# Optimization experiments

Measured on AMD Instinct MI355X. Metric: run time of the kernel, lower is better.

## Reference

```python
import jax, jax.numpy as jnp
import numpy as np

B, S, D, K = 64, 2048, 192, 128  # batch, seq, projection_dim, memoryBankSize


def setup_inputs() -> dict:
    key = jax.random.key(0)
    k1, k2, k3 = jax.random.split(key, 3)
    return {
        "projections": jax.random.normal(k1, (B, S, D), jnp.float32),
        "mem_bank": jax.random.normal(k2, (K, D), jnp.float32),
        "glu_w": jax.random.normal(k3, (D, 2 * D), jnp.float32) * 0.05,
        "glu_b": jnp.zeros((2 * D,), jnp.float32),
    }


def _l2_normalize(x, axis):
    # matches tf.math.l2_normalize (eps inside the max under the sqrt)
    sq = jnp.sum(x * x, axis=axis, keepdims=True)
    return x / jnp.sqrt(jnp.maximum(sq, 1e-12))


def _sinkhorn(out):
    # out: [K, N] cosine similarities
    Q = jnp.exp(out / 0.05)
    Kf = jnp.asarray(Q.shape[0], Q.dtype)
    Bf = jnp.asarray(Q.shape[1], Q.dtype)
    Q = Q / jnp.sum(Q)
    for _ in range(3):  # fixed 3 iterations, as in source
        Q = Q / (jnp.sum(Q, axis=1, keepdims=True) * Kf)  # row normalize
        Q = Q / (jnp.sum(Q, axis=0, keepdims=True) * Bf)  # col normalize
    return Q * Bf


def reference(projections, mem_bank, glu_w, glu_b):
    Bsz, Ssz, Dd = projections.shape
    x = projections.reshape(-1, Dd)                      # [N, D]
    proj_n = _l2_normalize(x, axis=1)                    # [N, D]
    mem_n = _l2_normalize(mem_bank, axis=1)              # [K, D]
    sim = jnp.einsum('kd,nd->kn', mem_n, proj_n)         # [K, N]
    Q = _sinkhorn(sim)                                   # [K, N]
    # top_k(Q^T, 1) per token == argmax over codebook axis
    idx = jnp.argmax(Q, axis=0)                          # [N] int
    assign = mem_bank[idx]                               # gather, [N, D]
    # GLU: Dense(2D) then value * sigmoid(gate)
    lin = assign @ glu_w + glu_b                         # [N, 2D]
    gated = lin[:, :Dd] * jax.nn.sigmoid(lin[:, Dd:])    # [N, D]
    # reduce_mean over the stacked pair == average
    return (projections + gated.reshape(Bsz, Ssz, Dd)) * 0.5
```

## Files before the change

### kernel.cpp

```cpp
#include <hip/hip_runtime.h>

#define NTOK  131072
#define DDIM  192
#define KMEM  128
#define TWOD  384
#define GBLK  2048

typedef _Float16 half8 __attribute__((ext_vector_type(8)));
typedef float   floatx4 __attribute__((ext_vector_type(4)));

__device__ __forceinline__ int swz(int row, int h) {
  return row * DDIM + ((((h >> 3) ^ (row & 7)) << 3));
}

__global__ __launch_bounds__(192) void prep_kernel(
    const float* __restrict__ mb, const float* __restrict__ W,
    const float* __restrict__ bias, _Float16* __restrict__ bhi,
    _Float16* __restrict__ blo, float* __restrict__ tab) {
  __shared__ float row[DDIM];
  __shared__ float red[DDIM];
  __shared__ float s_rn;
  const int k = blockIdx.x;
  const int t = threadIdx.x;
  float m = mb[k * DDIM + t];
  row[t] = m;
  red[t] = m * m;
  __syncthreads();
  if (t == 0) {
    float s = 0.f;
    for (int i = 0; i < DDIM; ++i) s += red[i];
    s_rn = 1.0f / sqrtf(fmaxf(s, 1e-12f));
  }
  __syncthreads();
  const float mn = m * s_rn;
  const _Float16 hh = (_Float16)mn;
  const float lo = (mn - (float)hh) * 4096.0f;
  bhi[k * DDIM + t] = hh;
  blo[k * DDIM + t] = (_Float16)lo;
  float a = bias[t], g = bias[DDIM + t];
  for (int d = 0; d < DDIM; ++d) {
    float r = row[d];
    a = fmaf(r, W[d * TWOD + t], a);
    g = fmaf(r, W[d * TWOD + DDIM + t], g);
  }
  float sg = 1.0f / (1.0f + expf(-g));
  tab[k * DDIM + t] = a * sg;
}

__global__ __launch_bounds__(256, 3) void sim_kernel(
    const float* __restrict__ proj, const _Float16* __restrict__ bhi_g,
    const _Float16* __restrict__ blo_g, float* __restrict__ E,
    double* __restrict__ Rp) {
  __shared__ _Float16 Ahi[64 * DDIM];
  __shared__ _Float16 Alo[64 * DDIM];
  __shared__ float rn_s[64];
  const int tid = threadIdx.x;
  const int lane = tid & 63;
  const int wid = tid >> 6;
  const long n0 = (long)blockIdx.x * 64;
  const int m_row = lane & 15;
  const int quad = lane >> 4;
  const int code_base = wid * 32;

  half8 bh[2][6], bl[2][6];
#pragma unroll
  for (int sn = 0; sn < 2; ++sn) {
    const int code = code_base + sn * 16 + m_row;
#pragma unroll
    for (int c = 0; c < 6; ++c) {
      const int gb = code * DDIM + c * 32 + quad * 8;
      bh[sn][c] = *(const half8*)&bhi_g[gb];
      bl[sn][c] = *(const half8*)&blo_g[gb];
    }
  }

  {
    const int row = tid >> 2;
    const int part = tid & 3;
    const float* src = &proj[(n0 + row) * DDIM + part * 48];
    float nsq = 0.f;
#pragma unroll
    for (int i = 0; i < 6; ++i) {
      float4 p0 = *(const float4*)(src + i * 8);
      float4 p1 = *(const float4*)(src + i * 8 + 4);
      float xs[8] = {p0.x, p0.y, p0.z, p0.w, p1.x, p1.y, p1.z, p1.w};
      half8 h, l;
#pragma unroll
      for (int j = 0; j < 8; ++j) {
        float x = xs[j];
        nsq = fmaf(x, x, nsq);
        _Float16 hh = (_Float16)x;
        h[j] = hh;
        l[j] = (_Float16)((x - (float)hh) * 4096.0f);
      }
      const int ha = swz(row, part * 48 + i * 8);
      *(half8*)&Ahi[ha] = h;
      *(half8*)&Alo[ha] = l;
    }
    nsq += __shfl_xor(nsq, 1);
    nsq += __shfl_xor(nsq, 2);
    if (part == 0) rn_s[row] = 1.0f / sqrtf(fmaxf(nsq, 1e-12f));
  }
  __syncthreads();

  float rcol[2] = {0.f, 0.f};
#pragma unroll
  for (int sm = 0; sm < 4; ++sm) {
    const int arow = sm * 16 + m_row;
    half8 ah[6], al[6];
#pragma unroll
    for (int c = 0; c < 6; ++c) {
      const int ha = swz(arow, c * 32 + quad * 8);
      ah[c] = *(const half8*)&Ahi[ha];
      al[c] = *(const half8*)&Alo[ha];
    }
    floatx4 a1[2], a2[2];
#pragma unroll
    for (int sn = 0; sn < 2; ++sn) {
      a1[sn] = (floatx4)0.0f;
      a2[sn] = (floatx4)0.0f;
#pragma unroll
      for (int c = 0; c < 6; ++c) {
        a1[sn] = __builtin_amdgcn_mfma_f32_16x16x32_f16(ah[c], bh[sn][c], a1[sn], 0, 0, 0);
        a2[sn] = __builtin_amdgcn_mfma_f32_16x16x32_f16(ah[c], bl[sn][c], a2[sn], 0, 0, 0);
        a2[sn] = __builtin_amdgcn_mfma_f32_16x16x32_f16(al[c], bh[sn][c], a2[sn], 0, 0, 0);
      }
    }
    float rnr[4];
#pragma unroll
    for (int r = 0; r < 4; ++r) rnr[r] = rn_s[sm * 16 + quad * 4 + r];
#pragma unroll
    for (int sn = 0; sn < 2; ++sn) {
      const int code = code_base + sn * 16 + m_row;
#pragma unroll
      for (int r = 0; r < 4; ++r) {
        const int tok = sm * 16 + quad * 4 + r;
        const float sim = fmaf(a2[sn][r], 0.000244140625f, a1[sn][r]) * rnr[r];
        const float e = expf(sim / 0.05f);
        E[(n0 + tok) * KMEM + code] = e;
        rcol[sn] += e;
      }
    }
  }
#pragma unroll
  for (int sn = 0; sn < 2; ++sn) {
    rcol[sn] += __shfl_xor(rcol[sn], 16);
    rcol[sn] += __shfl_xor(rcol[sn], 32);
  }
  if (lane < 16) {
    Rp[(long)blockIdx.x * KMEM + code_base + lane] = (double)rcol[0];
    Rp[(long)blockIdx.x * KMEM + code_base + 16 + lane] = (double)rcol[1];
  }
}

__global__ __launch_bounds__(256) void u_kernel(const double* __restrict__ Rp,
                                                float* __restrict__ u) {
  __shared__ double wred[4];
  const int k = blockIdx.x;
  const int t = threadIdx.x;
  double s = 0.0;
#pragma unroll
  for (int j = 0; j < GBLK / 256; ++j)
    s += Rp[(long)(j * 256 + t) * KMEM + k];
#pragma unroll
  for (int off = 1; off < 64; off <<= 1) s += __shfl_xor(s, off);
  if ((t & 63) == 0) wred[t >> 6] = s;
  __syncthreads();
  if (t == 0)
    u[k] = (float)(1.0 / (128.0 * (wred[0] + wred[1] + wred[2] + wred[3])));
}

__global__ __launch_bounds__(256) void cv_kernel(const float* __restrict__ E,
                                                 const float* __restrict__ u,
                                                 double* __restrict__ Rp) {
  __shared__ double part[4][KMEM];
  const int tid = threadIdx.x;
  const int l = tid & 7;
  const int ts = tid >> 3;
  const long n0 = (long)blockIdx.x * 64;
  float4 u4[4];
#pragma unroll
  for (int j = 0; j < 4; ++j) u4[j] = *(const float4*)&u[l * 16 + j * 4];
  double r[16];
#pragma unroll
  for (int i = 0; i < 16; ++i) r[i] = 0.0;
#pragma unroll
  for (int it = 0; it < 2; ++it) {
    const long n = n0 + it * 32 + ts;
    const float* Er = &E[n * KMEM + l * 16];
    const float4 e0 = *(const float4*)(Er + 0);
    const float4 e1 = *(const float4*)(Er + 4);
    const float4 e2 = *(const float4*)(Er + 8);
    const float4 e3 = *(const float4*)(Er + 12);
    double p0 = (double)e0.x * u4[0].x + (double)e0.y * u4[0].y;
    double p1 = (double)e0.z * u4[0].z + (double)e0.w * u4[0].w;
    double p2 = (double)e1.x * u4[1].x + (double)e1.y * u4[1].y;
    double p3 = (double)e1.z * u4[1].z + (double)e1.w * u4[1].w;
    double p4 = (double)e2.x * u4[2].x + (double)e2.y * u4[2].y;
    double p5 = (double)e2.z * u4[2].z + (double)e2.w * u4[2].w;
    double p6 = (double)e3.x * u4[3].x + (double)e3.y * u4[3].y;
    double p7 = (double)e3.z * u4[3].z + (double)e3.w * u4[3].w;
    double q0 = p0 + p1, q1 = p2 + p3, q2 = p4 + p5, q3 = p6 + p7;
    double c = (q0 + q1) + (q2 + q3);
    c += __shfl_xor(c, 1);
    c += __shfl_xor(c, 2);
    c += __shfl_xor(c, 4);
    const float v = (float)(1.0 / (131072.0 * c));
    r[0] += (double)(e0.x * v);
    r[1] += (double)(e0.y * v);
    r[2] += (double)(e0.z * v);
    r[3] += (double)(e0.w * v);
    r[4] += (double)(e1.x * v);
    r[5] += (double)(e1.y * v);
    r[6] += (double)(e1.z * v);
    r[7] += (double)(e1.w * v);
    r[8] += (double)(e2.x * v);
    r[9] += (double)(e2.y * v);
    r[10] += (double)(e2.z * v);
    r[11] += (double)(e2.w * v);
    r[12] += (double)(e3.x * v);
    r[13] += (double)(e3.y * v);
    r[14] += (double)(e3.z * v);
    r[15] += (double)(e3.w * v);
  }
#pragma unroll
  for (int i = 0; i < 16; ++i) {
    r[i] += __shfl_xor(r[i], 8);
    r[i] += __shfl_xor(r[i], 16);
    r[i] += __shfl_xor(r[i], 32);
  }
  if ((tid & 63) < 8) {
    const int w = tid >> 6;
#pragma unroll
    for (int i = 0; i < 16; ++i) part[w][l * 16 + i] = r[i];
  }
  __syncthreads();
  if (tid < KMEM) {
    const double s = part[0][tid] + part[1][tid] + part[2][tid] + part[3][tid];
    Rp[(long)blockIdx.x * KMEM + tid] = s;
  }
}

__global__ __launch_bounds__(256) void argmax_kernel(
    const float* __restrict__ E, const float* __restrict__ u,
    int* __restrict__ idx) {
  const int tid = threadIdx.x;
  const int l = tid & 7;
  const int ts = tid >> 3;
  const long n0 = (long)blockIdx.x * 64;
  float4 u4[4];
#pragma unroll
  for (int j = 0; j < 4; ++j) u4[j] = *(const float4*)&u[l * 16 + j * 4];
#pragma unroll
  for (int it = 0; it < 2; ++it) {
    const long n = n0 + it * 32 + ts;
    const float* Er = &E[n * KMEM + l * 16];
    const float4 e0 = *(const float4*)(Er + 0);
    const float4 e1 = *(const float4*)(Er + 4);
    const float4 e2 = *(const float4*)(Er + 8);
    const float4 e3 = *(const float4*)(Er + 12);
    float p[16];
    p[0] = e0.x * u4[0].x; p[1] = e0.y * u4[0].y;
    p[2] = e0.z * u4[0].z; p[3] = e0.w * u4[0].w;
    p[4] = e1.x * u4[1].x; p[5] = e1.y * u4[1].y;
    p[6] = e1.z * u4[1].z; p[7] = e1.w * u4[1].w;
    p[8] = e2.x * u4[2].x; p[9] = e2.y * u4[2].y;
    p[10] = e2.z * u4[2].z; p[11] = e2.w * u4[2].w;
    p[12] = e3.x * u4[3].x; p[13] = e3.y * u4[3].y;
    p[14] = e3.z * u4[3].z; p[15] = e3.w * u4[3].w;
    float bv = p[0];
    int bi = l * 16;
#pragma unroll
    for (int i = 1; i < 16; ++i) {
      if (p[i] > bv) { bv = p[i]; bi = l * 16 + i; }
    }
#pragma unroll
    for (int off = 1; off < 8; off <<= 1) {
      const float ov = __shfl_xor(bv, off);
      const int oi = __shfl_xor(bi, off);
      if (ov > bv || (ov == bv && oi < bi)) { bv = ov; bi = oi; }
    }
    if (l == 0) idx[n] = bi;
  }
}

__global__ __launch_bounds__(256) void out_kernel(
    const float* __restrict__ proj, const float* __restrict__ tab,
    const int* __restrict__ idx, float* __restrict__ out) {
  const long base = (long)blockIdx.x * 3072;
#pragma unroll
  for (int j = 0; j < 12; ++j) {
    const long f = base + j * 256 + threadIdx.x;
    const int t = (int)(f / 48);
    const int r = (int)(f - (long)t * 48);
    const int id = idx[t];
    const float4 p = *(const float4*)&proj[f * 4];
    const float4 tb = *(const float4*)&tab[id * DDIM + r * 4];
    float4 o;
    o.x = (p.x + tb.x) * 0.5f;
    o.y = (p.y + tb.y) * 0.5f;
    o.z = (p.z + tb.z) * 0.5f;
    o.w = (p.w + tb.w) * 0.5f;
    *(float4*)&out[f * 4] = o;
  }
}

extern "C" void kernel_launch(void* const* d_in, const int* in_sizes, int n_in,
                              void* d_out, int out_size, void* d_ws,
                              size_t ws_size, hipStream_t stream) {
  const float* proj = (const float*)d_in[0];
  const float* mb = (const float*)d_in[1];
  const float* W = (const float*)d_in[2];
  const float* bias = (const float*)d_in[3];
  float* out = (float*)d_out;
  char* ws = (char*)d_ws;
  float* tab = (float*)(ws);
  _Float16* bhi = (_Float16*)(ws + 98304);
  _Float16* blo = (_Float16*)(ws + 147456);
  float* u1 = (float*)(ws + 196608);
  float* u2 = (float*)(ws + 197120);
  float* u3 = (float*)(ws + 197632);
  int* idx = (int*)(ws + 198144);
  double* RpA = (double*)(ws + 722432);
  double* RpB = (double*)(ws + 2819584);
  float* E = out;

  prep_kernel<<<KMEM, DDIM, 0, stream>>>(mb, W, bias, bhi, blo, tab);
  sim_kernel<<<GBLK, 256, 0, stream>>>(proj, bhi, blo, E, RpA);
  u_kernel<<<KMEM, 256, 0, stream>>>(RpA, u1);
  cv_kernel<<<GBLK, 256, 0, stream>>>(E, u1, RpB);
  u_kernel<<<KMEM, 256, 0, stream>>>(RpB, u2);
  cv_kernel<<<GBLK, 256, 0, stream>>>(E, u2, RpA);
  u_kernel<<<KMEM, 256, 0, stream>>>(RpA, u3);
  argmax_kernel<<<GBLK, 256, 0, stream>>>(E, u3, idx);
  out_kernel<<<GBLK, 256, 0, stream>>>(proj, tab, idx, out);
}
```

Measured before the change: 308.3 us.

## Restructure sim kernel to per-wave token tiles and enlarge cv/argmax blocks

The similarity kernel no longer stages the projection tile in LDS. Each wave now owns 16 tokens, holds their hi/lo fp16 fragments in registers, and loops over all 8 code groups, reloading codebook fragments from global memory (expected to hit cache) on each iteration. Per-code partial sums are reduced across waves through a small LDS buffer. The cv and argmax kernels now process 128 tokens per block on half the grid, and u_kernel takes a runtime width. This removes the LDS staging and barrier cost, but adds repeated codebook reads per wave and changes the E store pattern.

```diff
diff --git a/kernel.cpp b/kernel.cpp
--- a/kernel.cpp
+++ b/kernel.cpp
@@ -4,14 +4,11 @@
 #define DDIM  192
 #define KMEM  128
 #define TWOD  384
-#define GBLK  2048
+#define SIMGRID 2048
+#define CVGRID  1024
 
 typedef _Float16 half8 __attribute__((ext_vector_type(8)));
 typedef float   floatx4 __attribute__((ext_vector_type(4)));
-
-__device__ __forceinline__ int swz(int row, int h) {
-  return row * DDIM + ((((h >> 3) ^ (row & 7)) << 3));
-}
 
 __global__ __launch_bounds__(192) void prep_kernel(
     const float* __restrict__ mb, const float* __restrict__ W,
@@ -51,117 +48,96 @@
     const float* __restrict__ proj, const _Float16* __restrict__ bhi_g,
     const _Float16* __restrict__ blo_g, float* __restrict__ E,
     double* __restrict__ Rp) {
-  __shared__ _Float16 Ahi[64 * DDIM];
-  __shared__ _Float16 Alo[64 * DDIM];
-  __shared__ float rn_s[64];
+  __shared__ double red_s[4][KMEM];
   const int tid = threadIdx.x;
   const int lane = tid & 63;
   const int wid = tid >> 6;
-  const long n0 = (long)blockIdx.x * 64;
   const int m_row = lane & 15;
   const int quad = lane >> 4;
-  const int code_base = wid * 32;
-
-  half8 bh[2][6], bl[2][6];
-#pragma unroll
-  for (int sn = 0; sn < 2; ++sn) {
-    const int code = code_base + sn * 16 + m_row;
+  const long tile = (long)blockIdx.x * 4 + wid;
+  const long n0 = tile * 16;
+
+  float4 raw[12];
+  const float* abase = &proj[(n0 + m_row) * DDIM + quad * 8];
+#pragma unroll
+  for (int c = 0; c < 6; ++c) {
+    raw[2 * c] = *(const float4*)(abase + c * 32);
+    raw[2 * c + 1] = *(const float4*)(abase + c * 32 + 4);
+  }
+  half8 ah[6], al[6];
+  float nsq = 0.f;
+#pragma unroll
+  for (int c = 0; c < 6; ++c) {
+    float xs[8] = {raw[2 * c].x,     raw[2 * c].y,     raw[2 * c].z,
+                   raw[2 * c].w,     raw[2 * c + 1].x, raw[2 * c + 1].y,
+                   raw[2 * c + 1].z, raw[2 * c + 1].w};
+    half8 h, l;
+#pragma unroll
+    for (int j = 0; j < 8; ++j) {
+      float x = xs[j];
+      nsq = fmaf(x, x, nsq);
+      _Float16 hh = (_Float16)x;
+      h[j] = hh;
+      l[j] = (_Float16)((x - (float)hh) * 4096.0f);
+    }
+    ah[c] = h;
+    al[c] = l;
+  }
+  nsq += __shfl_xor(nsq, 16);
+  nsq += __shfl_xor(nsq, 32);
+  const float rn = 1.0f / sqrtf(fmaxf(nsq, 1e-12f));
+  float rnr[4];
+#pragma unroll
+  for (int r = 0; r < 4; ++r) rnr[r] = __shfl(rn, quad * 4 + r);
+
+#pragma unroll 1
+  for (int sn = 0; sn < 8; ++sn) {
+    const int code = sn * 16 + m_row;
+    const _Float16* bb = &bhi_g[code * DDIM + quad * 8];
+    const _Float16* lb = &blo_g[code * DDIM + quad * 8];
+    half8 bh[6], bl[6];
 #pragma unroll
     for (int c = 0; c < 6; ++c) {
-      const int gb = code * DDIM + c * 32 + quad * 8;
-      bh[sn][c] = *(const half8*)&bhi_g[gb];
-      bl[sn][c] = *(const half8*)&blo_g[gb];
-    }
-  }
-
-  {
-    const int row = tid >> 2;
-    const int part = tid & 3;
-    const float* src = &proj[(n0 + row) * DDIM + part * 48];
-    float nsq = 0.f;
-#pragma unroll
-    for (int i = 0; i < 6; ++i) {
-      float4 p0 = *(const float4*)(src + i * 8);
-      float4 p1 = *(const float4*)(src + i * 8 + 4);
-      float xs[8] = {p0.x, p0.y, p0.z, p0.w, p1.x, p1.y, p1.z, p1.w};
-      half8 h, l;
-#pragma unroll
-      for (int j = 0; j < 8; ++j) {
-        float x = xs[j];
-        nsq = fmaf(x, x, nsq);
-        _Float16 hh = (_Float16)x;
-        h[j] = hh;
-        l[j] = (_Float16)((x - (float)hh) * 4096.0f);
-      }
-      const int ha = swz(row, part * 48 + i * 8);
-      *(half8*)&Ahi[ha] = h;
-      *(half8*)&Alo[ha] = l;
-    }
-    nsq += __shfl_xor(nsq, 1);
-    nsq += __shfl_xor(nsq, 2);
-    if (part == 0) rn_s[row] = 1.0f / sqrtf(fmaxf(nsq, 1e-12f));
-  }
-  __syncthreads();
-
-  float rcol[2] = {0.f, 0.f};
-#pragma unroll
-  for (int sm = 0; sm < 4; ++sm) {
-    const int arow = sm * 16 + m_row;
-    half8 ah[6], al[6];
+      bh[c] = *(const half8*)(bb + c * 32);
+      bl[c] = *(const half8*)(lb + c * 32);
+    }
+    floatx4 a1 = (floatx4)0.0f;
+    floatx4 a2 = (floatx4)0.0f;
 #pragma unroll
     for (int c = 0; c < 6; ++c) {
-      const int ha = swz(arow, c * 32 + quad * 8);
-      ah[c] = *(const half8*)&Ahi[ha];
-      al[c] = *(const half8*)&Alo[ha];
-    }
-    floatx4 a1[2], a2[2];
-#pragma unroll
-    for (int sn = 0; sn < 2; ++sn) {
-      a1[sn] = (floatx4)0.0f;
-      a2[sn] = (floatx4)0.0f;
-#pragma unroll
-      for (int c = 0; c < 6; ++c) {
-        a1[sn] = __builtin_amdgcn_mfma_f32_16x16x32_f16(ah[c], bh[sn][c], a1[sn], 0, 0, 0);
-        a2[sn] = __builtin_amdgcn_mfma_f32_16x16x32_f16(ah[c], bl[sn][c], a2[sn], 0, 0, 0);
-        a2[sn] = __builtin_amdgcn_mfma_f32_16x16x32_f16(al[c], bh[sn][c], a2[sn], 0, 0, 0);
-      }
-    }
-    float rnr[4];
-#pragma unroll
-    for (int r = 0; r < 4; ++r) rnr[r] = rn_s[sm * 16 + quad * 4 + r];
-#pragma unroll
-    for (int sn = 0; sn < 2; ++sn) {
-      const int code = code_base + sn * 16 + m_row;
-#pragma unroll
-      for (int r = 0; r < 4; ++r) {
-        const int tok = sm * 16 + quad * 4 + r;
-        const float sim = fmaf(a2[sn][r], 0.000244140625f, a1[sn][r]) * rnr[r];
-        const float e = expf(sim / 0.05f);
-        E[(n0 + tok) * KMEM + code] = e;
-        rcol[sn] += e;
-      }
-    }
-  }
-#pragma unroll
-  for (int sn = 0; sn < 2; ++sn) {
-    rcol[sn] += __shfl_xor(rcol[sn], 16);
-    rcol[sn] += __shfl_xor(rcol[sn], 32);
-  }
-  if (lane < 16) {
-    Rp[(long)blockIdx.x * KMEM + code_base + lane] = (double)rcol[0];
-    Rp[(long)blockIdx.x * KMEM + code_base + 16 + lane] = (double)rcol[1];
+      a1 = __builtin_amdgcn_mfma_f32_16x16x32_f16(ah[c], bh[c], a1, 0, 0, 0);
+      a2 = __builtin_amdgcn_mfma_f32_16x16x32_f16(ah[c], bl[c], a2, 0, 0, 0);
+      a2 = __builtin_amdgcn_mfma_f32_16x16x32_f16(al[c], bh[c], a2, 0, 0, 0);
+    }
+    float rcol = 0.f;
+#pragma unroll
+    for (int r = 0; r < 4; ++r) {
+      const int tok = quad * 4 + r;
+      const float sim = fmaf(a2[r], 0.000244140625f, a1[r]) * rnr[r];
+      const float e = expf(sim / 0.05f);
+      E[(n0 + tok) * KMEM + code] = e;
+      rcol += e;
+    }
+    rcol += __shfl_xor(rcol, 16);
+    rcol += __shfl_xor(rcol, 32);
+    if (lane < 16) red_s[wid][code] = (double)rcol;
+  }
+  __syncthreads();
+  if (tid < KMEM) {
+    const double s =
+        red_s[0][tid] + red_s[1][tid] + red_s[2][tid] + red_s[3][tid];
+    Rp[(long)blockIdx.x * KMEM + tid] = s;
   }
 }
 
 __global__ __launch_bounds__(256) void u_kernel(const double* __restrict__ Rp,
-                                                float* __restrict__ u) {
+                                                float* __restrict__ u,
+                                                int width) {
   __shared__ double wred[4];
   const int k = blockIdx.x;
   const int t = threadIdx.x;
   double s = 0.0;
-#pragma unroll
-  for (int j = 0; j < GBLK / 256; ++j)
-    s += Rp[(long)(j * 256 + t) * KMEM + k];
+  for (int j = t; j < width; j += 256) s += Rp[(long)j * KMEM + k];
 #pragma unroll
   for (int off = 1; off < 64; off <<= 1) s += __shfl_xor(s, off);
   if ((t & 63) == 0) wred[t >> 6] = s;
@@ -177,7 +153,7 @@
   const int tid = threadIdx.x;
   const int l = tid & 7;
   const int ts = tid >> 3;
-  const long n0 = (long)blockIdx.x * 64;
+  const long n0 = (long)blockIdx.x * 128;
   float4 u4[4];
 #pragma unroll
   for (int j = 0; j < 4; ++j) u4[j] = *(const float4*)&u[l * 16 + j * 4];
@@ -185,7 +161,7 @@
 #pragma unroll
   for (int i = 0; i < 16; ++i) r[i] = 0.0;
 #pragma unroll
-  for (int it = 0; it < 2; ++it) {
+  for (int it = 0; it < 4; ++it) {
     const long n = n0 + it * 32 + ts;
     const float* Er = &E[n * KMEM + l * 16];
     const float4 e0 = *(const float4*)(Er + 0);
@@ -247,12 +223,12 @@
   const int tid = threadIdx.x;
   const int l = tid & 7;
   const int ts = tid >> 3;
-  const long n0 = (long)blockIdx.x * 64;
+  const long n0 = (long)blockIdx.x * 128;
   float4 u4[4];
 #pragma unroll
   for (int j = 0; j < 4; ++j) u4[j] = *(const float4*)&u[l * 16 + j * 4];
 #pragma unroll
-  for (int it = 0; it < 2; ++it) {
+  for (int it = 0; it < 4; ++it) {
     const long n = n0 + it * 32 + ts;
     const float* Er = &E[n * KMEM + l * 16];
     const float4 e0 = *(const float4*)(Er + 0);
@@ -326,12 +302,12 @@
   float* E = out;
 
   prep_kernel<<<KMEM, DDIM, 0, stream>>>(mb, W, bias, bhi, blo, tab);
-  sim_kernel<<<GBLK, 256, 0, stream>>>(proj, bhi, blo, E, RpA);
-  u_kernel<<<KMEM, 256, 0, stream>>>(RpA, u1);
-  cv_kernel<<<GBLK, 256, 0, stream>>>(E, u1, RpB);
-  u_kernel<<<KMEM, 256, 0, stream>>>(RpB, u2);
-  cv_kernel<<<GBLK, 256, 0, stream>>>(E, u2, RpA);
-  u_kernel<<<KMEM, 256, 0, stream>>>(RpA, u3);
-  argmax_kernel<<<GBLK, 256, 0, stream>>>(E, u3, idx);
-  out_kernel<<<GBLK, 256, 0, stream>>>(proj, tab, idx, out);
-}
+  sim_kernel<<<SIMGRID, 256, 0, stream>>>(proj, bhi, blo, E, RpA);
+  u_kernel<<<KMEM, 256, 0, stream>>>(RpA, u1, SIMGRID);
+  cv_kernel<<<CVGRID, 256, 0, stream>>>(E, u1, RpB);
+  u_kernel<<<KMEM, 256, 0, stream>>>(RpB, u2, CVGRID);
+  cv_kernel<<<CVGRID, 256, 0, stream>>>(E, u2, RpB);
+  u_kernel<<<KMEM, 256, 0, stream>>>(RpB, u3, CVGRID);
+  argmax_kernel<<<CVGRID, 256, 0, stream>>>(E, u3, idx);
+  out_kernel<<<SIMGRID, 256, 0, stream>>>(proj, tab, idx, out);
+}
```

Result: slower. 342.2 us (+11.0%).
